# Kernel tuning notes

Hardware: AMD Instinct MI355X
Metric: run time of the kernel (lower is better)

The kernel has to match this reference:

```python
import jax, jax.numpy as jnp
import numpy as np

KSIZE = 3  # module init kwarg


def setup_inputs() -> dict:
    key = jax.random.key(0)
    k1, k2, k3 = jax.random.split(key, 3)
    shape = (16, 3, 512, 512)  # [B, C, H, W]
    return {
        "sr": jax.random.normal(k1, shape, jnp.float32),
        "sr_ema": jax.random.normal(k2, shape, jnp.float32),
        "hr": jax.random.normal(k3, shape, jnp.float32),
    }


def _local_var(res, ksize):
    """Unbiased variance over a ksize x ksize sliding window with reflect pad.

    Matches torch: reflect-pad then unfold + var(unbiased=True). Implemented as a
    box-filter over sum and sum-of-squares (no ksize^2-larger unfold tensor).
    res: [B, 1, H, W] -> [B, 1, H, W]
    """
    pad = (ksize - 1) // 2
    rp = jnp.pad(res, ((0, 0), (0, 0), (pad, pad), (pad, pad)), mode="reflect")
    n = ksize * ksize
    win = (1, 1, ksize, ksize)
    strides = (1, 1, 1, 1)
    zero = jnp.zeros((), rp.dtype)
    s = jax.lax.reduce_window(rp, zero, jax.lax.add, win, strides, "VALID")
    sq = jax.lax.reduce_window(rp * rp, zero, jax.lax.add, win, strides, "VALID")
    # unbiased: (sum(x^2) - sum(x)^2/n) / (n-1)
    return (sq - s * s / n) / (n - 1)


def reference(sr, sr_ema, hr):
    # per-pixel channel-summed residuals, [B, 1, H, W]
    residual_ema = jnp.sum(jnp.abs(hr - sr_ema), axis=1, keepdims=True) / 255.0
    residual_sr = jnp.sum(jnp.abs(hr - sr), axis=1, keepdims=True) / 255.0

    r_det = jax.lax.stop_gradient(residual_sr)  # .clone().detach() in torch

    # patch-level weight: unbiased var over (C=1, H, W) per sample, ** (1/5)
    n_patch = r_det.shape[1] * r_det.shape[2] * r_det.shape[3]
    mean = jnp.mean(r_det, axis=(-1, -2, -3), keepdims=True)
    patch_var = jnp.sum((r_det - mean) ** 2, axis=(-1, -2, -3), keepdims=True) / (n_patch - 1)
    patch_w = patch_var ** 0.2  # [B,1,1,1]

    pixel_w = _local_var(r_det, KSIZE)  # [B,1,H,W]

    overall_w = patch_w * pixel_w
    overall_w = jnp.where(residual_sr < residual_ema, jnp.zeros((), overall_w.dtype), overall_w)

    # L1 loss (mean reduction) between weighted sr and weighted hr
    return jnp.mean(jnp.abs(overall_w * sr - overall_w * hr))
```

## Files before the change

kernel.cpp:

```cpp
#include <hip/hip_runtime.h>
#include <math.h>


#define BB 16
#define HH 512
#define WW 512
#define HW (HH * WW)
#define CHW (3 * HW)
#define TILES_PER_BATCH 64
#define NBLOCKS (BB * TILES_PER_BATCH)
#define LDS_STRIDE 264

__device__ __forceinline__ int reflect_h(int gh) {
  gh = gh < 0 ? -gh : gh;
  return gh >= HH ? 2 * HH - 2 - gh : gh;
}

__global__ __launch_bounds__(256) void wl1_main(
    const float* __restrict__ sr, const float* __restrict__ srema,
    const float* __restrict__ hr,
    float* __restrict__ p_sum, float* __restrict__ p_sum2,
    float* __restrict__ p_loss) {
  __shared__ float rt[18][LDS_STRIDE];
  const int bid = blockIdx.x;
  const int b = bid >> 6;
  const int t = bid & 63;
  const int h0 = (t >> 1) << 4;
  const int w0 = (t & 1) << 8;
  const int tid = threadIdx.x;
  const int c4 = tid & 63;
  const int rs = tid >> 6;
  const float* __restrict__ srb = sr + (size_t)b * CHW;
  const float* __restrict__ hrb = hr + (size_t)b * CHW;
  const float* __restrict__ eb = srema + (size_t)b * CHW;

#pragma unroll
  for (int it = 0; it < 5; ++it) {
    int row = it * 4 + rs;
    if (row < 18) {
      int gh = reflect_h(h0 - 1 + row);
      const float* hb = hrb + gh * WW + w0 + 4 * c4;
      const float* sb = srb + gh * WW + w0 + 4 * c4;
      float4 ha = *(const float4*)(hb);
      float4 hbv = *(const float4*)(hb + HW);
      float4 hc = *(const float4*)(hb + 2 * HW);
      float4 sa = *(const float4*)(sb);
      float4 sbv = *(const float4*)(sb + HW);
      float4 sc = *(const float4*)(sb + 2 * HW);
      float4 r4;
      r4.x = (fabsf(ha.x - sa.x) + fabsf(hbv.x - sbv.x) + fabsf(hc.x - sc.x)) / 255.0f;
      r4.y = (fabsf(ha.y - sa.y) + fabsf(hbv.y - sbv.y) + fabsf(hc.y - sc.y)) / 255.0f;
      r4.z = (fabsf(ha.z - sa.z) + fabsf(hbv.z - sbv.z) + fabsf(hc.z - sc.z)) / 255.0f;
      r4.w = (fabsf(ha.w - sa.w) + fabsf(hbv.w - sbv.w) + fabsf(hc.w - sc.w)) / 255.0f;
      *(float4*)&rt[row][4 + 4 * c4] = r4;
    }
  }
  if (tid < 36) {
    int row = tid >> 1, side = tid & 1;
    int gh = reflect_h(h0 - 1 + row);
    int gw = side ? w0 + 256 : w0 - 1;
    if (gw < 0) gw = 1;
    if (gw > 511) gw = 1022 - gw;
    int base = gh * WW + gw;
    float v = (fabsf(hrb[base] - srb[base]) +
               fabsf(hrb[base + HW] - srb[base + HW]) +
               fabsf(hrb[base + 2 * HW] - srb[base + 2 * HW])) /
              255.0f;
    rt[row][side ? 260 : 3] = v;
  }
  __syncthreads();

  float v1 = 0.f, v2 = 0.f, v3 = 0.f;
  const int row0 = rs * 4;
#pragma unroll
  for (int rr = 0; rr < 4; ++rr) {
    const int orow = row0 + rr;
    float cs[6] = {0, 0, 0, 0, 0, 0}, cq[6] = {0, 0, 0, 0, 0, 0};
    float center[4];
#pragma unroll
    for (int dr = 0; dr < 3; ++dr) {
      const float* lp = &rt[orow + dr][4 * c4];
      float4 a = *(const float4*)(lp);
      float4 bq = *(const float4*)(lp + 4);
      float4 cq4 = *(const float4*)(lp + 8);
      float f3 = a.w, f4 = bq.x, f5 = bq.y, f6 = bq.z, f7 = bq.w, f8 = cq4.x;
      cs[0] += f3; cq[0] += f3 * f3;
      cs[1] += f4; cq[1] += f4 * f4;
      cs[2] += f5; cq[2] += f5 * f5;
      cs[3] += f6; cq[3] += f6 * f6;
      cs[4] += f7; cq[4] += f7 * f7;
      cs[5] += f8; cq[5] += f8 * f8;
      if (dr == 1) { center[0] = f4; center[1] = f5; center[2] = f6; center[3] = f7; }
    }
    const int gbase = (h0 + orow) * WW + w0 + 4 * c4;
    float4 ha = *(const float4*)(hrb + gbase);
    float4 hb2 = *(const float4*)(hrb + gbase + HW);
    float4 hc = *(const float4*)(hrb + gbase + 2 * HW);
    float4 ea = *(const float4*)(eb + gbase);
    float4 eb2 = *(const float4*)(eb + gbase + HW);
    float4 ec = *(const float4*)(eb + gbase + 2 * HW);
    float e4[4];
    e4[0] = (fabsf(ha.x - ea.x) + fabsf(hb2.x - eb2.x) + fabsf(hc.x - ec.x)) / 255.0f;
    e4[1] = (fabsf(ha.y - ea.y) + fabsf(hb2.y - eb2.y) + fabsf(hc.y - ec.y)) / 255.0f;
    e4[2] = (fabsf(ha.z - ea.z) + fabsf(hb2.z - eb2.z) + fabsf(hc.z - ec.z)) / 255.0f;
    e4[3] = (fabsf(ha.w - ea.w) + fabsf(hb2.w - eb2.w) + fabsf(hc.w - ec.w)) / 255.0f;
#pragma unroll
    for (int cc = 0; cc < 4; ++cc) {
      float s = cs[cc] + cs[cc + 1] + cs[cc + 2];
      float q = cq[cc] + cq[cc + 1] + cq[cc + 2];
      float pvar = (q - s * s / 9.0f) / 8.0f;
      float rc = center[cc];
      v1 += rc;
      v2 += rc * rc;
      if (rc >= e4[cc]) v3 += pvar * (255.0f * rc);
    }
  }

#pragma unroll
  for (int off = 32; off > 0; off >>= 1) {
    v1 += __shfl_down(v1, off, 64);
    v2 += __shfl_down(v2, off, 64);
    v3 += __shfl_down(v3, off, 64);
  }
  __shared__ float red[3][4];
  if (c4 == 0) {
    red[0][rs] = v1;
    red[1][rs] = v2;
    red[2][rs] = v3;
  }
  __syncthreads();
  if (tid == 0) {
    p_sum[bid] = red[0][0] + red[0][1] + red[0][2] + red[0][3];
    p_sum2[bid] = red[1][0] + red[1][1] + red[1][2] + red[1][3];
    p_loss[bid] = red[2][0] + red[2][1] + red[2][2] + red[2][3];
  }
}

__global__ __launch_bounds__(1024) void wl1_reduce(
    const float* __restrict__ p_sum, const float* __restrict__ p_sum2,
    const float* __restrict__ p_loss, float* __restrict__ out) {
  const int tid = threadIdx.x;
  const int b = tid >> 6, k = tid & 63;
  const int i = b * TILES_PER_BATCH + k;
  double s = (double)p_sum[i], s2 = (double)p_sum2[i], sl = (double)p_loss[i];
#pragma unroll
  for (int off = 32; off > 0; off >>= 1) {
    s += __shfl_down(s, off, 64);
    s2 += __shfl_down(s2, off, 64);
    sl += __shfl_down(sl, off, 64);
  }
  __shared__ double acc[BB];
  if (k == 0) {
    const double n = (double)HW;
    double var = (s2 - s * s / n) / (n - 1.0);
    acc[b] = pow(var, 0.2) * sl;
  }
  __syncthreads();
  if (tid == 0) {
    double tot = 0.0;
#pragma unroll
    for (int j = 0; j < BB; ++j) tot += acc[j];
    out[0] = (float)(tot / (double)((size_t)BB * CHW));
  }
}

extern "C" void kernel_launch(void* const* d_in, const int* in_sizes, int n_in,
                              void* d_out, int out_size, void* d_ws,
                              size_t ws_size, hipStream_t stream) {
  const float* sr = (const float*)d_in[0];
  const float* srema = (const float*)d_in[1];
  const float* hr = (const float*)d_in[2];
  float* out = (float*)d_out;

  float* p_sum = (float*)d_ws;
  float* p_sum2 = p_sum + NBLOCKS;
  float* p_loss = p_sum2 + NBLOCKS;

  wl1_main<<<NBLOCKS, 256, 0, stream>>>(sr, srema, hr, p_sum, p_sum2, p_loss);
  wl1_reduce<<<1, 1024, 0, stream>>>(p_sum, p_sum2, p_loss, out);
}
```

Measured before the change: 159.0 us.

## Replace LDS tile with per-wave register sliding window over row strips

Each wave now processes an 8-row strip of 256 columns and keeps a rolling window of three residual rows in registers. Horizontal neighbours are exchanged with wave shuffles instead of going through shared memory, which removes the LDS tile and both block barriers. Each row's hr data is loaded once and reused for the sr and sr_ema residuals. The smaller strips raise the halo fraction: each strip re-reads 2 halo rows per 8 output rows, versus 2 per 16 before. The reduce kernel now loops over more partials per batch.

```diff
diff --git a/kernel.cpp b/kernel.cpp
--- a/kernel.cpp
+++ b/kernel.cpp
@@ -7,113 +7,131 @@
 #define WW 512
 #define HW (HH * WW)
 #define CHW (3 * HW)
-#define TILES_PER_BATCH 64
-#define NBLOCKS (BB * TILES_PER_BATCH)
-#define LDS_STRIDE 264
+#define STRIP 8
+#define NSTRIPS (HH / STRIP)
+#define REG_PER_B (2 * NSTRIPS)
+#define NREGIONS (BB * REG_PER_B)
+#define NBLOCKS (NREGIONS / 4)
 
 __device__ __forceinline__ int reflect_h(int gh) {
   gh = gh < 0 ? -gh : gh;
   return gh >= HH ? 2 * HH - 2 - gh : gh;
 }
 
+struct Row {
+  float4 r;
+  float4 e;
+  float lv, rv;
+};
+
+template <bool WITH_E>
+__device__ __forceinline__ Row load_row(const float* __restrict__ hrb,
+                                        const float* __restrict__ srb,
+                                        const float* __restrict__ emb, int n,
+                                        int col, int wedge, bool edge_lane,
+                                        int lane) {
+  Row o;
+  const int gh = reflect_h(n);
+  const float* hp = hrb + gh * WW + col;
+  const float* sp = srb + gh * WW + col;
+  float4 h0 = *(const float4*)hp;
+  float4 h1 = *(const float4*)(hp + HW);
+  float4 h2 = *(const float4*)(hp + 2 * HW);
+  float4 s0 = *(const float4*)sp;
+  float4 s1 = *(const float4*)(sp + HW);
+  float4 s2 = *(const float4*)(sp + 2 * HW);
+  o.r.x = (fabsf(h0.x - s0.x) + fabsf(h1.x - s1.x) + fabsf(h2.x - s2.x)) / 255.0f;
+  o.r.y = (fabsf(h0.y - s0.y) + fabsf(h1.y - s1.y) + fabsf(h2.y - s2.y)) / 255.0f;
+  o.r.z = (fabsf(h0.z - s0.z) + fabsf(h1.z - s1.z) + fabsf(h2.z - s2.z)) / 255.0f;
+  o.r.w = (fabsf(h0.w - s0.w) + fabsf(h1.w - s1.w) + fabsf(h2.w - s2.w)) / 255.0f;
+  if (WITH_E) {
+    const float* ep = emb + gh * WW + col;
+    float4 e0 = *(const float4*)ep;
+    float4 e1 = *(const float4*)(ep + HW);
+    float4 e2 = *(const float4*)(ep + 2 * HW);
+    o.e.x = (fabsf(h0.x - e0.x) + fabsf(h1.x - e1.x) + fabsf(h2.x - e2.x)) / 255.0f;
+    o.e.y = (fabsf(h0.y - e0.y) + fabsf(h1.y - e1.y) + fabsf(h2.y - e2.y)) / 255.0f;
+    o.e.z = (fabsf(h0.z - e0.z) + fabsf(h1.z - e1.z) + fabsf(h2.z - e2.z)) / 255.0f;
+    o.e.w = (fabsf(h0.w - e0.w) + fabsf(h1.w - e1.w) + fabsf(h2.w - e2.w)) / 255.0f;
+  } else {
+    o.e = make_float4(0.f, 0.f, 0.f, 0.f);
+  }
+  float edge = 0.f;
+  if (edge_lane) {
+    const float* hq = hrb + gh * WW + wedge;
+    const float* sq = srb + gh * WW + wedge;
+    edge = (fabsf(hq[0] - sq[0]) + fabsf(hq[HW] - sq[HW]) +
+            fabsf(hq[2 * HW] - sq[2 * HW])) /
+           255.0f;
+  }
+  float lvs = __shfl_up(o.r.w, 1, 64);
+  float rvs = __shfl_down(o.r.x, 1, 64);
+  o.lv = (lane == 0) ? edge : lvs;
+  o.rv = (lane == 63) ? edge : rvs;
+  return o;
+}
+
+__device__ __forceinline__ void row6(const Row& R, float* v) {
+  v[0] = R.lv; v[1] = R.r.x; v[2] = R.r.y; v[3] = R.r.z; v[4] = R.r.w; v[5] = R.rv;
+}
+
 __global__ __launch_bounds__(256) void wl1_main(
     const float* __restrict__ sr, const float* __restrict__ srema,
-    const float* __restrict__ hr,
-    float* __restrict__ p_sum, float* __restrict__ p_sum2,
-    float* __restrict__ p_loss) {
-  __shared__ float rt[18][LDS_STRIDE];
-  const int bid = blockIdx.x;
-  const int b = bid >> 6;
-  const int t = bid & 63;
-  const int h0 = (t >> 1) << 4;
-  const int w0 = (t & 1) << 8;
+    const float* __restrict__ hr, float* __restrict__ p_sum,
+    float* __restrict__ p_sum2, float* __restrict__ p_loss) {
   const int tid = threadIdx.x;
-  const int c4 = tid & 63;
-  const int rs = tid >> 6;
+  const int lane = tid & 63;
+  const int region = blockIdx.x * 4 + (tid >> 6);
+  const int b = region >> 7;
+  const int rem = region & 127;
+  const int w0 = (rem & 1) << 8;
+  const int h0 = (rem >> 1) * STRIP;
+
   const float* __restrict__ srb = sr + (size_t)b * CHW;
   const float* __restrict__ hrb = hr + (size_t)b * CHW;
-  const float* __restrict__ eb = srema + (size_t)b * CHW;
+  const float* __restrict__ emb = srema + (size_t)b * CHW;
 
-#pragma unroll
-  for (int it = 0; it < 5; ++it) {
-    int row = it * 4 + rs;
-    if (row < 18) {
-      int gh = reflect_h(h0 - 1 + row);
-      const float* hb = hrb + gh * WW + w0 + 4 * c4;
-      const float* sb = srb + gh * WW + w0 + 4 * c4;
-      float4 ha = *(const float4*)(hb);
-      float4 hbv = *(const float4*)(hb + HW);
-      float4 hc = *(const float4*)(hb + 2 * HW);
-      float4 sa = *(const float4*)(sb);
-      float4 sbv = *(const float4*)(sb + HW);
-      float4 sc = *(const float4*)(sb + 2 * HW);
-      float4 r4;
-      r4.x = (fabsf(ha.x - sa.x) + fabsf(hbv.x - sbv.x) + fabsf(hc.x - sc.x)) / 255.0f;
-      r4.y = (fabsf(ha.y - sa.y) + fabsf(hbv.y - sbv.y) + fabsf(hc.y - sc.y)) / 255.0f;
-      r4.z = (fabsf(ha.z - sa.z) + fabsf(hbv.z - sbv.z) + fabsf(hc.z - sc.z)) / 255.0f;
-      r4.w = (fabsf(ha.w - sa.w) + fabsf(hbv.w - sbv.w) + fabsf(hc.w - sc.w)) / 255.0f;
-      *(float4*)&rt[row][4 + 4 * c4] = r4;
-    }
-  }
-  if (tid < 36) {
-    int row = tid >> 1, side = tid & 1;
-    int gh = reflect_h(h0 - 1 + row);
-    int gw = side ? w0 + 256 : w0 - 1;
-    if (gw < 0) gw = 1;
-    if (gw > 511) gw = 1022 - gw;
-    int base = gh * WW + gw;
-    float v = (fabsf(hrb[base] - srb[base]) +
-               fabsf(hrb[base + HW] - srb[base + HW]) +
-               fabsf(hrb[base + 2 * HW] - srb[base + 2 * HW])) /
-              255.0f;
-    rt[row][side ? 260 : 3] = v;
-  }
-  __syncthreads();
+  const int col = w0 + 4 * lane;
+  const int wl = (w0 == 0) ? 1 : w0 - 1;
+  const int wrr = (w0 + 256 >= WW) ? (2 * WW - 2 - (w0 + 256)) : (w0 + 256);
+  const bool edge_lane = (lane == 0) || (lane == 63);
+  const int wedge = (lane == 0) ? wl : wrr;
+
+  Row A = load_row<false>(hrb, srb, emb, h0 - 1, col, wedge, edge_lane, lane);
+  Row B = load_row<true>(hrb, srb, emb, h0, col, wedge, edge_lane, lane);
+  Row C = load_row<true>(hrb, srb, emb, h0 + 1, col, wedge, edge_lane, lane);
 
   float v1 = 0.f, v2 = 0.f, v3 = 0.f;
-  const int row0 = rs * 4;
 #pragma unroll
-  for (int rr = 0; rr < 4; ++rr) {
-    const int orow = row0 + rr;
-    float cs[6] = {0, 0, 0, 0, 0, 0}, cq[6] = {0, 0, 0, 0, 0, 0};
-    float center[4];
+  for (int i = 0; i < STRIP; ++i) {
+    Row D = C;
+    if (i + 2 < STRIP) {
+      D = load_row<true>(hrb, srb, emb, h0 + i + 2, col, wedge, edge_lane, lane);
+    } else if (i + 2 == STRIP) {
+      D = load_row<false>(hrb, srb, emb, h0 + i + 2, col, wedge, edge_lane, lane);
+    }
+
+    float vA[6], vB[6], vC[6];
+    row6(A, vA); row6(B, vB); row6(C, vC);
+    float cs[6], cq[6];
 #pragma unroll
-    for (int dr = 0; dr < 3; ++dr) {
-      const float* lp = &rt[orow + dr][4 * c4];
-      float4 a = *(const float4*)(lp);
-      float4 bq = *(const float4*)(lp + 4);
-      float4 cq4 = *(const float4*)(lp + 8);
-      float f3 = a.w, f4 = bq.x, f5 = bq.y, f6 = bq.z, f7 = bq.w, f8 = cq4.x;
-      cs[0] += f3; cq[0] += f3 * f3;
-      cs[1] += f4; cq[1] += f4 * f4;
-      cs[2] += f5; cq[2] += f5 * f5;
-      cs[3] += f6; cq[3] += f6 * f6;
-      cs[4] += f7; cq[4] += f7 * f7;
-      cs[5] += f8; cq[5] += f8 * f8;
-      if (dr == 1) { center[0] = f4; center[1] = f5; center[2] = f6; center[3] = f7; }
+    for (int j = 0; j < 6; ++j) {
+      cs[j] = vA[j] + vB[j] + vC[j];
+      cq[j] = vA[j] * vA[j] + vB[j] * vB[j] + vC[j] * vC[j];
     }
-    const int gbase = (h0 + orow) * WW + w0 + 4 * c4;
-    float4 ha = *(const float4*)(hrb + gbase);
-    float4 hb2 = *(const float4*)(hrb + gbase + HW);
-    float4 hc = *(const float4*)(hrb + gbase + 2 * HW);
-    float4 ea = *(const float4*)(eb + gbase);
-    float4 eb2 = *(const float4*)(eb + gbase + HW);
-    float4 ec = *(const float4*)(eb + gbase + 2 * HW);
-    float e4[4];
-    e4[0] = (fabsf(ha.x - ea.x) + fabsf(hb2.x - eb2.x) + fabsf(hc.x - ec.x)) / 255.0f;
-    e4[1] = (fabsf(ha.y - ea.y) + fabsf(hb2.y - eb2.y) + fabsf(hc.y - ec.y)) / 255.0f;
-    e4[2] = (fabsf(ha.z - ea.z) + fabsf(hb2.z - eb2.z) + fabsf(hc.z - ec.z)) / 255.0f;
-    e4[3] = (fabsf(ha.w - ea.w) + fabsf(hb2.w - eb2.w) + fabsf(hc.w - ec.w)) / 255.0f;
+    const float rcv[4] = {B.r.x, B.r.y, B.r.z, B.r.w};
+    const float ev[4] = {B.e.x, B.e.y, B.e.z, B.e.w};
 #pragma unroll
-    for (int cc = 0; cc < 4; ++cc) {
-      float s = cs[cc] + cs[cc + 1] + cs[cc + 2];
-      float q = cq[cc] + cq[cc + 1] + cq[cc + 2];
+    for (int c = 0; c < 4; ++c) {
+      float s = cs[c] + cs[c + 1] + cs[c + 2];
+      float q = cq[c] + cq[c + 1] + cq[c + 2];
       float pvar = (q - s * s / 9.0f) / 8.0f;
-      float rc = center[cc];
+      float rc = rcv[c];
       v1 += rc;
       v2 += rc * rc;
-      if (rc >= e4[cc]) v3 += pvar * (255.0f * rc);
+      if (rc >= ev[c]) v3 += pvar * (255.0f * rc);
     }
+    A = B; B = C; C = D;
   }
 
 #pragma unroll
@@ -122,17 +140,10 @@
     v2 += __shfl_down(v2, off, 64);
     v3 += __shfl_down(v3, off, 64);
   }
-  __shared__ float red[3][4];
-  if (c4 == 0) {
-    red[0][rs] = v1;
-    red[1][rs] = v2;
-    red[2][rs] = v3;
-  }
-  __syncthreads();
-  if (tid == 0) {
-    p_sum[bid] = red[0][0] + red[0][1] + red[0][2] + red[0][3];
-    p_sum2[bid] = red[1][0] + red[1][1] + red[1][2] + red[1][3];
-    p_loss[bid] = red[2][0] + red[2][1] + red[2][2] + red[2][3];
+  if (lane == 0) {
+    p_sum[region] = v1;
+    p_sum2[region] = v2;
+    p_loss[region] = v3;
   }
 }
 
@@ -141,8 +152,14 @@
     const float* __restrict__ p_loss, float* __restrict__ out) {
   const int tid = threadIdx.x;
   const int b = tid >> 6, k = tid & 63;
-  const int i = b * TILES_PER_BATCH + k;
-  double s = (double)p_sum[i], s2 = (double)p_sum2[i], sl = (double)p_loss[i];
+  double s = 0.0, s2 = 0.0, sl = 0.0;
+#pragma unroll
+  for (int j = 0; j < REG_PER_B; j += 64) {
+    int i = b * REG_PER_B + j + k;
+    s += (double)p_sum[i];
+    s2 += (double)p_sum2[i];
+    sl += (double)p_loss[i];
+  }
 #pragma unroll
   for (int off = 32; off > 0; off >>= 1) {
     s += __shfl_down(s, off, 64);
@@ -173,8 +190,8 @@
   float* out = (float*)d_out;
 
   float* p_sum = (float*)d_ws;
-  float* p_sum2 = p_sum + NBLOCKS;
-  float* p_loss = p_sum2 + NBLOCKS;
+  float* p_sum2 = p_sum + NREGIONS;
+  float* p_loss = p_sum2 + NREGIONS;
 
   wl1_main<<<NBLOCKS, 256, 0, stream>>>(sr, srema, hr, p_sum, p_sum2, p_loss);
   wl1_reduce<<<1, 1024, 0, stream>>>(p_sum, p_sum2, p_loss, out);
```

Result: slower. 173.4 us (+9.1%).
